# Performance work log

Hardware: AMD Instinct MI355X
Metric: run time of the kernel (lower is better)

The kernel has to match this reference:

```python
import jax, jax.numpy as jnp
import numpy as np

BITS = 4
MAXQ = 15            # 2**BITS - 1
PACK = 32 // BITS    # 8 int4 values per int32
GROUPSIZE = 128
M, K, N = 2048, 4096, 4096
G = K // GROUPSIZE


def setup_inputs() -> dict:
    key = jax.random.key(0)
    k1, k2, k3, k4, k5 = jax.random.split(key, 5)
    x = jax.random.normal(k1, (M, K), dtype=jnp.float32)
    qweight = jax.random.randint(k2, (K // PACK, N), 0, 2147483647, dtype=jnp.int32)
    qzeros = jax.random.randint(k3, (G, N // PACK), 0, 2147483647, dtype=jnp.int32)
    scales = jax.random.uniform(k4, (G, N), dtype=jnp.float32) * 0.01
    g_idx = (jnp.arange(K, dtype=jnp.int32) // GROUPSIZE).astype(jnp.int32)
    bias = jax.random.normal(k5, (N,), dtype=jnp.float32)
    return {"x": x, "qweight": qweight, "qzeros": qzeros,
            "scales": scales, "g_idx": g_idx, "bias": bias}


def _dequantize(qweight, qzeros, scales, g_idx):
    shifts = (jnp.arange(PACK, dtype=jnp.int32) * BITS)
    # unpack weights along K: [K//8, N] -> [K//8, 8, N] -> [K, N]
    w_int = ((qweight[:, None, :] >> shifts[None, :, None]) & MAXQ)
    w_int = w_int.reshape(K, N)
    # unpack zeros along N: [G, N//8] -> [G, N//8, 8] -> [G, N]; kernel adds 1
    z_int = ((qzeros[:, :, None] >> shifts[None, None, :]) & MAXQ) + 1
    z_int = z_int.reshape(G, N)
    # group-wise dequant: W[k, n] = (w - zeros[g_idx[k]]) * scales[g_idx[k]]
    W = (w_int - z_int[g_idx]).astype(jnp.float32) * scales[g_idx]
    return W  # [K, N]


def reference(x, qweight, qzeros, scales, g_idx, bias):
    W = _dequantize(qweight, qzeros, scales, g_idx)
    return x @ W + bias  # [M, N]
```

## Files before the change

kernel.cpp:

```cpp
#include <hip/hip_runtime.h>
#include <hip/hip_bf16.h>
#include <stdint.h>

#define M_DIM 2048
#define K_DIM 4096
#define N_DIM 4096

typedef __attribute__((ext_vector_type(8))) short short8;
typedef __attribute__((ext_vector_type(4))) float f32x4;

__device__ __forceinline__ uint32_t bf16pk(float a, float b) {
  uint32_t ua = __float_as_uint(a);
  ua = (ua + 0x7FFFu + ((ua >> 16) & 1u)) >> 16;
  uint32_t ub = __float_as_uint(b);
  ub = (ub + 0x7FFFu + ((ub >> 16) & 1u)) >> 16;
  return ua | (ub << 16);
}

__device__ __forceinline__ void glds16(const char* g, char* l) {
  __builtin_amdgcn_global_load_lds((__attribute__((address_space(1))) void*)g,
                                   (__attribute__((address_space(3))) void*)l, 16, 0, 0);
}


__global__ void __launch_bounds__(256) cvt_x_kernel(const float* __restrict__ x,
                                                    char* __restrict__ xImg) {
  const int mt = blockIdx.x >> 6, kt = blockIdx.x & 63;
  const int tid = threadIdx.x;
  const int k8 = tid & 7, rbase = tid >> 3;
  const float* xb = x + (size_t)mt * 256 * K_DIM + kt * 64 + k8 * 8;
  char* ob = xImg + (size_t)(mt * 64 + kt) * 32768 + k8 * 4096;
#pragma unroll
  for (int j = 0; j < 8; ++j) {
    int row = j * 32 + rbase;
    const float* src = xb + (size_t)row * K_DIM;
    float4 f0 = *(const float4*)src;
    float4 f1 = *(const float4*)(src + 4);
    uint4 pk;
    pk.x = bf16pk(f0.x, f0.y);
    pk.y = bf16pk(f0.z, f0.w);
    pk.z = bf16pk(f1.x, f1.y);
    pk.w = bf16pk(f1.z, f1.w);
    *(uint4*)(ob + row * 16) = pk;
  }
}

__global__ void __launch_bounds__(256) deq_w_kernel(const uint32_t* __restrict__ qweight,
                                                    const uint32_t* __restrict__ qzeros,
                                                    const float* __restrict__ scales,
                                                    char* __restrict__ wImg) {
  const int nt = blockIdx.x >> 6, kt = blockIdx.x & 63;
  const int t = threadIdx.x;
  const int n = nt * 256 + t;
  const int g = kt >> 1;
  uint32_t zq = qzeros[g * (N_DIM / 8) + (n >> 3)];
  const int z = (int)((zq >> ((n & 7) * 4)) & 15u) + 1;
  const float s = scales[g * N_DIM + n];
  char* ob = wImg + (size_t)(nt * 64 + kt) * 32768;
#pragma unroll
  for (int slot = 0; slot < 8; ++slot) {
    uint32_t q = qweight[(size_t)(kt * 8 + slot) * N_DIM + n];
    float f[8];
#pragma unroll
    for (int v = 0; v < 8; ++v) {
      int w = (int)((q >> (4 * v)) & 15u);
      f[v] = (float)(w - z) * s;
    }
    uint4 pk;
    pk.x = bf16pk(f[0], f[1]);
    pk.y = bf16pk(f[2], f[3]);
    pk.z = bf16pk(f[4], f[5]);
    pk.w = bf16pk(f[6], f[7]);
    *(uint4*)(ob + slot * 4096 + t * 16) = pk;
  }
}

__global__ void __launch_bounds__(512, 2) gemm_kernel(const char* __restrict__ xImg,
                                                      const char* __restrict__ wImg,
                                                      const float* __restrict__ bias,
                                                      float* __restrict__ out,
                                                      float* __restrict__ part1) {
  __shared__ uint4 ldsv[8192];
  char* lds = (char*)ldsv;
  const int tid = threadIdx.x;
  const int lane = tid & 63, wid = tid >> 6;
  const int wr = wid >> 2, wc = wid & 3;
  const int lr = lane & 15, lk = lane >> 4;

  const int bid = blockIdx.x;
  const int i5 = bid >> 3;
  const int nb = (bid & 7) * 2 + (i5 & 1);
  const int mb = (i5 >> 1) & 7;
  const int ks = i5 >> 4;

  f32x4 acc[8][4];
#pragma unroll
  for (int i = 0; i < 8; ++i)
#pragma unroll
    for (int j = 0; j < 4; ++j) acc[i][j] = f32x4{0.f, 0.f, 0.f, 0.f};

  const char* aT = xImg + (size_t)(mb * 64 + ks * 32) * 32768;
  const char* bT = wImg + (size_t)(nb * 64 + ks * 32) * 32768;

  int aoff[8], boff[4];
#pragma unroll
  for (int i = 0; i < 8; ++i) aoff[i] = lk * 4096 + (wr * 128 + i * 16 + lr) * 16;
#pragma unroll
  for (int j = 0; j < 4; ++j) boff[j] = 32768 + lk * 4096 + (wc * 64 + j * 16 + lr) * 16;

#define STG(src, off)                                        \
  do {                                                       \
    glds16((src) + tid * 16, lds + (off) + tid * 16);        \
    glds16((src) + 8192 + tid * 16, lds + (off) + 8192 + tid * 16); \
  } while (0)

  STG(aT, 0);
  STG(bT, 32768);
  STG(aT + 16384, 16384);
  STG(bT + 16384, 49152);
  STG(aT + 32768, 65536);
  STG(bT + 32768, 65536 + 32768);

#pragma unroll 2
  for (int t = 0; t < 32; ++t) {
    const int c = t & 1;
    char* bufc = lds + c * 65536;
    char* bufn = lds + (c ^ 1) * 65536;
    const char* aN1 = aT + (size_t)(t + 1) * 32768;
    const char* bN1 = bT + (size_t)(t + 1) * 32768;
    const char* aN2 = aT + (size_t)(t + 2) * 32768;
    const char* bN2 = bT + (size_t)(t + 2) * 32768;
    short8 a[8], b0, b1, b2, b3;

    if (t == 31) asm volatile("s_waitcnt vmcnt(4)" ::: "memory");
    else         asm volatile("s_waitcnt vmcnt(8)" ::: "memory");
    __builtin_amdgcn_sched_barrier(0);
    __builtin_amdgcn_s_barrier();
    if (t < 31) STG(aN1 + 16384, (c ^ 1) * 65536 + 16384);
#pragma unroll
    for (int i = 0; i < 8; ++i) a[i] = *(const short8*)(bufc + aoff[i]);
    b0 = *(const short8*)(bufc + boff[0]);
    b1 = *(const short8*)(bufc + boff[1]);
    __builtin_amdgcn_s_setprio(1);
#pragma unroll
    for (int i = 0; i < 8; ++i) {
      acc[i][0] = __builtin_amdgcn_mfma_f32_16x16x32_bf16(a[i], b0, acc[i][0], 0, 0, 0);
      acc[i][1] = __builtin_amdgcn_mfma_f32_16x16x32_bf16(a[i], b1, acc[i][1], 0, 0, 0);
    }
    __builtin_amdgcn_s_setprio(0);

    __builtin_amdgcn_s_barrier();
    if (t < 31) STG(bN1 + 16384, (c ^ 1) * 65536 + 32768 + 16384);
    b2 = *(const short8*)(bufc + boff[2]);
    b3 = *(const short8*)(bufc + boff[3]);
    __builtin_amdgcn_s_setprio(1);
#pragma unroll
    for (int i = 0; i < 8; ++i) {
      acc[i][2] = __builtin_amdgcn_mfma_f32_16x16x32_bf16(a[i], b2, acc[i][2], 0, 0, 0);
      acc[i][3] = __builtin_amdgcn_mfma_f32_16x16x32_bf16(a[i], b3, acc[i][3], 0, 0, 0);
    }
    __builtin_amdgcn_s_setprio(0);

    if (t == 31) asm volatile("s_waitcnt vmcnt(0)" ::: "memory");
    else         asm volatile("s_waitcnt vmcnt(8)" ::: "memory");
    __builtin_amdgcn_sched_barrier(0);
    __builtin_amdgcn_s_barrier();
    if (t < 30) STG(aN2, c * 65536);
#pragma unroll
    for (int i = 0; i < 8; ++i) a[i] = *(const short8*)(bufc + aoff[i] + 16384);
    b0 = *(const short8*)(bufc + boff[0] + 16384);
    b1 = *(const short8*)(bufc + boff[1] + 16384);
    __builtin_amdgcn_s_setprio(1);
#pragma unroll
    for (int i = 0; i < 8; ++i) {
      acc[i][0] = __builtin_amdgcn_mfma_f32_16x16x32_bf16(a[i], b0, acc[i][0], 0, 0, 0);
      acc[i][1] = __builtin_amdgcn_mfma_f32_16x16x32_bf16(a[i], b1, acc[i][1], 0, 0, 0);
    }
    __builtin_amdgcn_s_setprio(0);

    __builtin_amdgcn_s_barrier();
    if (t < 30) STG(bN2, c * 65536 + 32768);
    b2 = *(const short8*)(bufc + boff[2] + 16384);
    b3 = *(const short8*)(bufc + boff[3] + 16384);
    __builtin_amdgcn_s_setprio(1);
#pragma unroll
    for (int i = 0; i < 8; ++i) {
      acc[i][2] = __builtin_amdgcn_mfma_f32_16x16x32_bf16(a[i], b2, acc[i][2], 0, 0, 0);
      acc[i][3] = __builtin_amdgcn_mfma_f32_16x16x32_bf16(a[i], b3, acc[i][3], 0, 0, 0);
    }
    __builtin_amdgcn_s_setprio(0);
  }
#undef STG

  const int colB = nb * 256 + wc * 64 + lr;
  const int rowB = mb * 256 + wr * 128 + lk * 4;
  if (part1 != nullptr) {
    float* dst = ks ? part1 : out;
#pragma unroll
    for (int j = 0; j < 4; ++j) {
      int col = colB + j * 16;
      float bj = (ks == 0) ? bias[col] : 0.f;
#pragma unroll
      for (int i = 0; i < 8; ++i) {
        int row = rowB + i * 16;
#pragma unroll
        for (int r = 0; r < 4; ++r)
          dst[(size_t)(row + r) * N_DIM + col] = acc[i][j][r] + bj;
      }
    }
  } else {
#pragma unroll
    for (int j = 0; j < 4; ++j) {
      int col = colB + j * 16;
      float bj = (ks == 0) ? bias[col] : 0.f;
#pragma unroll
      for (int i = 0; i < 8; ++i) {
        int row = rowB + i * 16;
#pragma unroll
        for (int r = 0; r < 4; ++r)
          atomicAdd(&out[(size_t)(row + r) * N_DIM + col], acc[i][j][r] + bj);
      }
    }
  }
}

__global__ void __launch_bounds__(256) reduce_kernel(float* __restrict__ out,
                                                     const float* __restrict__ part1) {
  int i = blockIdx.x * 256 + threadIdx.x;
  float4 o = ((const float4*)out)[i];
  float4 p = ((const float4*)part1)[i];
  o.x += p.x; o.y += p.y; o.z += p.z; o.w += p.w;
  ((float4*)out)[i] = o;
}

__global__ void fallback_kernel(const float* __restrict__ x, const uint32_t* __restrict__ qweight,
                                const uint32_t* __restrict__ qzeros, const float* __restrict__ scales,
                                const float* __restrict__ bias, float* __restrict__ out) {
  __shared__ float xs[16][17];
  __shared__ float ws[16][17];
  int tx = threadIdx.x, ty = threadIdx.y;
  int col = blockIdx.x * 16 + tx;
  int row = blockIdx.y * 16 + ty;
  float acc = 0.f;
  for (int k0 = 0; k0 < K_DIM; k0 += 16) {
    xs[ty][tx] = x[(size_t)row * K_DIM + k0 + tx];
    int k = k0 + ty;
    int g = k >> 7;
    uint32_t q = qweight[(size_t)(k >> 3) * N_DIM + col];
    int w = (int)((q >> ((k & 7) * 4)) & 15u);
    uint32_t zq = qzeros[g * (N_DIM / 8) + (col >> 3)];
    int z = (int)((zq >> ((col & 7) * 4)) & 15u) + 1;
    ws[ty][tx] = (float)(w - z) * scales[g * N_DIM + col];
    __syncthreads();
#pragma unroll
    for (int kk = 0; kk < 16; ++kk) acc += xs[ty][kk] * ws[kk][tx];
    __syncthreads();
  }
  out[(size_t)row * N_DIM + col] = acc + bias[col];
}

extern "C" void kernel_launch(void* const* d_in, const int* in_sizes, int n_in,
                              void* d_out, int out_size, void* d_ws, size_t ws_size,
                              hipStream_t stream) {
  const float* x = (const float*)d_in[0];
  const uint32_t* qweight = (const uint32_t*)d_in[1];
  const uint32_t* qzeros = (const uint32_t*)d_in[2];
  const float* scales = (const float*)d_in[3];
  const float* bias = (const float*)d_in[5];
  float* out = (float*)d_out;

  const size_t X_IMG = (size_t)8 * 64 * 32768;
  const size_t W_IMG = (size_t)16 * 64 * 32768;
  const size_t PART = (size_t)M_DIM * N_DIM * 4;

  if (ws_size >= X_IMG + W_IMG + PART) {
    char* xImg = (char*)d_ws;
    char* wImg = (char*)d_ws + X_IMG;
    float* part1 = (float*)((char*)d_ws + X_IMG + W_IMG);
    cvt_x_kernel<<<512, 256, 0, stream>>>(x, xImg);
    deq_w_kernel<<<1024, 256, 0, stream>>>(qweight, qzeros, scales, wImg);
    gemm_kernel<<<256, 512, 0, stream>>>(xImg, wImg, bias, out, part1);
    reduce_kernel<<<8192, 256, 0, stream>>>(out, part1);
  } else if (ws_size >= X_IMG + W_IMG) {
    char* xImg = (char*)d_ws;
    char* wImg = (char*)d_ws + X_IMG;
    hipMemsetAsync(out, 0, (size_t)M_DIM * N_DIM * sizeof(float), stream);
    cvt_x_kernel<<<512, 256, 0, stream>>>(x, xImg);
    deq_w_kernel<<<1024, 256, 0, stream>>>(qweight, qzeros, scales, wImg);
    gemm_kernel<<<256, 512, 0, stream>>>(xImg, wImg, bias, out, nullptr);
  } else {
    fallback_kernel<<<dim3(N_DIM / 16, M_DIM / 16), dim3(16, 16), 0, stream>>>(
        x, qweight, qzeros, scales, bias, out);
  }
}
```

Baseline: 96.87 us.

## Restructure GEMM main loop into four-stage LDS ring with register-prefetched fragments

```diff
diff --git a/kernel.cpp b/kernel.cpp
--- a/kernel.cpp
+++ b/kernel.cpp
@@ -8,6 +8,8 @@
 
 typedef __attribute__((ext_vector_type(8))) short short8;
 typedef __attribute__((ext_vector_type(4))) float f32x4;
+
+#define MFMA __builtin_amdgcn_mfma_f32_16x16x32_bf16
 
 __device__ __forceinline__ uint32_t bf16pk(float a, float b) {
   uint32_t ua = __float_as_uint(a);
@@ -99,96 +101,115 @@
 #pragma unroll
     for (int j = 0; j < 4; ++j) acc[i][j] = f32x4{0.f, 0.f, 0.f, 0.f};
 
-  const char* aT = xImg + (size_t)(mb * 64 + ks * 32) * 32768;
-  const char* bT = wImg + (size_t)(nb * 64 + ks * 32) * 32768;
+  const char* aT = xImg + (size_t)(mb * 128 + ks * 64) * 16384;
+  const char* bT = wImg + (size_t)(nb * 128 + ks * 64) * 16384;
 
   int aoff[8], boff[4];
 #pragma unroll
   for (int i = 0; i < 8; ++i) aoff[i] = lk * 4096 + (wr * 128 + i * 16 + lr) * 16;
 #pragma unroll
-  for (int j = 0; j < 4; ++j) boff[j] = 32768 + lk * 4096 + (wc * 64 + j * 16 + lr) * 16;
-
-#define STG(src, off)                                        \
-  do {                                                       \
-    glds16((src) + tid * 16, lds + (off) + tid * 16);        \
-    glds16((src) + 8192 + tid * 16, lds + (off) + 8192 + tid * 16); \
+  for (int j = 0; j < 4; ++j) boff[j] = 16384 + lk * 4096 + (wc * 64 + j * 16 + lr) * 16;
+
+#define STG(src, dstoff)                                                 \
+  do {                                                                   \
+    glds16((src) + tid * 16, lds + (dstoff) + tid * 16);                 \
+    glds16((src) + 8192 + tid * 16, lds + (dstoff) + 8192 + tid * 16);   \
   } while (0)
 
-  STG(aT, 0);
-  STG(bT, 32768);
-  STG(aT + 16384, 16384);
-  STG(bT + 16384, 49152);
-  STG(aT + 32768, 65536);
-  STG(bT + 32768, 65536 + 32768);
-
-#pragma unroll 2
-  for (int t = 0; t < 32; ++t) {
-    const int c = t & 1;
-    char* bufc = lds + c * 65536;
-    char* bufn = lds + (c ^ 1) * 65536;
-    const char* aN1 = aT + (size_t)(t + 1) * 32768;
-    const char* bN1 = bT + (size_t)(t + 1) * 32768;
-    const char* aN2 = aT + (size_t)(t + 2) * 32768;
-    const char* bN2 = bT + (size_t)(t + 2) * 32768;
-    short8 a[8], b0, b1, b2, b3;
-
-    if (t == 31) asm volatile("s_waitcnt vmcnt(4)" ::: "memory");
-    else         asm volatile("s_waitcnt vmcnt(8)" ::: "memory");
+  STG(aT, 0);                STG(bT, 16384);
+  STG(aT + 16384, 32768);    STG(bT + 16384, 32768 + 16384);
+  STG(aT + 32768, 65536);    STG(bT + 32768, 65536 + 16384);
+  asm volatile("s_waitcnt vmcnt(8)" ::: "memory");
+  __builtin_amdgcn_sched_barrier(0);
+  __builtin_amdgcn_s_barrier();
+
+  short8 a0 = *(const short8*)(lds + aoff[0]);
+  short8 a1 = *(const short8*)(lds + aoff[1]);
+  short8 a2 = *(const short8*)(lds + aoff[2]);
+  short8 a3 = *(const short8*)(lds + aoff[3]);
+  short8 b0 = *(const short8*)(lds + boff[0]);
+  short8 b1 = *(const short8*)(lds + boff[1]);
+
+#pragma unroll 4
+  for (int t = 0; t < 64; ++t) {
+    const char* buf  = lds + (t & 3) * 32768;
+    const char* bufn = lds + ((t + 1) & 3) * 32768;
+    const int nso = ((t + 3) & 3) * 32768;
+    const char* aN = aT + (size_t)(t + 3) * 16384;
+    const char* bN = bT + (size_t)(t + 3) * 16384;
+
+    short8 b2 = *(const short8*)(buf + boff[2]);
+    short8 b3 = *(const short8*)(buf + boff[3]);
+    short8 a4 = *(const short8*)(buf + aoff[4]);
+    short8 a5 = *(const short8*)(buf + aoff[5]);
+    short8 a6 = *(const short8*)(buf + aoff[6]);
+    short8 a7 = *(const short8*)(buf + aoff[7]);
+    if (t <= 60) STG(aN, nso);
     __builtin_amdgcn_sched_barrier(0);
     __builtin_amdgcn_s_barrier();
-    if (t < 31) STG(aN1 + 16384, (c ^ 1) * 65536 + 16384);
-#pragma unroll
-    for (int i = 0; i < 8; ++i) a[i] = *(const short8*)(bufc + aoff[i]);
-    b0 = *(const short8*)(bufc + boff[0]);
-    b1 = *(const short8*)(bufc + boff[1]);
+    asm volatile("s_waitcnt lgkmcnt(6)" ::: "memory");
+    __builtin_amdgcn_sched_barrier(0);
     __builtin_amdgcn_s_setprio(1);
-#pragma unroll
-    for (int i = 0; i < 8; ++i) {
-      acc[i][0] = __builtin_amdgcn_mfma_f32_16x16x32_bf16(a[i], b0, acc[i][0], 0, 0, 0);
-      acc[i][1] = __builtin_amdgcn_mfma_f32_16x16x32_bf16(a[i], b1, acc[i][1], 0, 0, 0);
-    }
+    acc[0][0] = MFMA(a0, b0, acc[0][0], 0, 0, 0);
+    acc[1][0] = MFMA(a1, b0, acc[1][0], 0, 0, 0);
+    acc[2][0] = MFMA(a2, b0, acc[2][0], 0, 0, 0);
+    acc[3][0] = MFMA(a3, b0, acc[3][0], 0, 0, 0);
+    acc[0][1] = MFMA(a0, b1, acc[0][1], 0, 0, 0);
+    acc[1][1] = MFMA(a1, b1, acc[1][1], 0, 0, 0);
+    acc[2][1] = MFMA(a2, b1, acc[2][1], 0, 0, 0);
+    acc[3][1] = MFMA(a3, b1, acc[3][1], 0, 0, 0);
+    asm volatile("s_waitcnt lgkmcnt(4)" ::: "memory");
+    __builtin_amdgcn_sched_barrier(0);
+    acc[0][2] = MFMA(a0, b2, acc[0][2], 0, 0, 0);
+    acc[1][2] = MFMA(a1, b2, acc[1][2], 0, 0, 0);
+    acc[2][2] = MFMA(a2, b2, acc[2][2], 0, 0, 0);
+    acc[3][2] = MFMA(a3, b2, acc[3][2], 0, 0, 0);
+    acc[0][3] = MFMA(a0, b3, acc[0][3], 0, 0, 0);
+    acc[1][3] = MFMA(a1, b3, acc[1][3], 0, 0, 0);
+    acc[2][3] = MFMA(a2, b3, acc[2][3], 0, 0, 0);
+    acc[3][3] = MFMA(a3, b3, acc[3][3], 0, 0, 0);
     __builtin_amdgcn_s_setprio(0);
-
+    if (t <= 60)      asm volatile("s_waitcnt vmcnt(6)" ::: "memory");
+    else if (t == 61) asm volatile("s_waitcnt vmcnt(4)" ::: "memory");
+    else if (t == 62) asm volatile("s_waitcnt vmcnt(0)" ::: "memory");
+    __builtin_amdgcn_sched_barrier(0);
     __builtin_amdgcn_s_barrier();
-    if (t < 31) STG(bN1 + 16384, (c ^ 1) * 65536 + 32768 + 16384);
-    b2 = *(const short8*)(bufc + boff[2]);
-    b3 = *(const short8*)(bufc + boff[3]);
+    __builtin_amdgcn_sched_barrier(0);
+
+    short8 na0 = *(const short8*)(bufn + aoff[0]);
+    short8 na1 = *(const short8*)(bufn + aoff[1]);
+    short8 na2 = *(const short8*)(bufn + aoff[2]);
+    short8 na3 = *(const short8*)(bufn + aoff[3]);
+    short8 nb0 = *(const short8*)(bufn + boff[0]);
+    short8 nb1 = *(const short8*)(bufn + boff[1]);
+    if (t <= 60) STG(bN, nso + 16384);
+    __builtin_amdgcn_sched_barrier(0);
+    __builtin_amdgcn_s_barrier();
+    asm volatile("s_waitcnt lgkmcnt(6)" ::: "memory");
+    __builtin_amdgcn_sched_barrier(0);
     __builtin_amdgcn_s_setprio(1);
-#pragma unroll
-    for (int i = 0; i < 8; ++i) {
-      acc[i][2] = __builtin_amdgcn_mfma_f32_16x16x32_bf16(a[i], b2, acc[i][2], 0, 0, 0);
-      acc[i][3] = __builtin_amdgcn_mfma_f32_16x16x32_bf16(a[i], b3, acc[i][3], 0, 0, 0);
-    }
+    acc[4][0] = MFMA(a4, b0, acc[4][0], 0, 0, 0);
+    acc[5][0] = MFMA(a5, b0, acc[5][0], 0, 0, 0);
+    acc[6][0] = MFMA(a6, b0, acc[6][0], 0, 0, 0);
+    acc[7][0] = MFMA(a7, b0, acc[7][0], 0, 0, 0);
+    acc[4][1] = MFMA(a4, b1, acc[4][1], 0, 0, 0);
+    acc[5][1] = MFMA(a5, b1, acc[5][1], 0, 0, 0);
+    acc[6][1] = MFMA(a6, b1, acc[6][1], 0, 0, 0);
+    acc[7][1] = MFMA(a7, b1, acc[7][1], 0, 0, 0);
+    acc[4][2] = MFMA(a4, b2, acc[4][2], 0, 0, 0);
+    acc[5][2] = MFMA(a5, b2, acc[5][2], 0, 0, 0);
+    acc[6][2] = MFMA(a6, b2, acc[6][2], 0, 0, 0);
+    acc[7][2] = MFMA(a7, b2, acc[7][2], 0, 0, 0);
+    acc[4][3] = MFMA(a4, b3, acc[4][3], 0, 0, 0);
+    acc[5][3] = MFMA(a5, b3, acc[5][3], 0, 0, 0);
+    acc[6][3] = MFMA(a6, b3, acc[6][3], 0, 0, 0);
+    acc[7][3] = MFMA(a7, b3, acc[7][3], 0, 0, 0);
     __builtin_amdgcn_s_setprio(0);
-
-    if (t == 31) asm volatile("s_waitcnt vmcnt(0)" ::: "memory");
-    else         asm volatile("s_waitcnt vmcnt(8)" ::: "memory");
     __builtin_amdgcn_sched_barrier(0);
     __builtin_amdgcn_s_barrier();
-    if (t < 30) STG(aN2, c * 65536);
-#pragma unroll
-    for (int i = 0; i < 8; ++i) a[i] = *(const short8*)(bufc + aoff[i] + 16384);
-    b0 = *(const short8*)(bufc + boff[0] + 16384);
-    b1 = *(const short8*)(bufc + boff[1] + 16384);
-    __builtin_amdgcn_s_setprio(1);
-#pragma unroll
-    for (int i = 0; i < 8; ++i) {
-      acc[i][0] = __builtin_amdgcn_mfma_f32_16x16x32_bf16(a[i], b0, acc[i][0], 0, 0, 0);
-      acc[i][1] = __builtin_amdgcn_mfma_f32_16x16x32_bf16(a[i], b1, acc[i][1], 0, 0, 0);
-    }
-    __builtin_amdgcn_s_setprio(0);
-
-    __builtin_amdgcn_s_barrier();
-    if (t < 30) STG(bN2, c * 65536 + 32768);
-    b2 = *(const short8*)(bufc + boff[2] + 16384);
-    b3 = *(const short8*)(bufc + boff[3] + 16384);
-    __builtin_amdgcn_s_setprio(1);
-#pragma unroll
-    for (int i = 0; i < 8; ++i) {
-      acc[i][2] = __builtin_amdgcn_mfma_f32_16x16x32_bf16(a[i], b2, acc[i][2], 0, 0, 0);
-      acc[i][3] = __builtin_amdgcn_mfma_f32_16x16x32_bf16(a[i], b3, acc[i][3], 0, 0, 0);
-    }
-    __builtin_amdgcn_s_setprio(0);
+    __builtin_amdgcn_sched_barrier(0);
+
+    a0 = na0; a1 = na1; a2 = na2; a3 = na3; b0 = nb0; b1 = nb1;
   }
 #undef STG
 
@@ -279,7 +300,7 @@
     float* part1 = (float*)((char*)d_ws + X_IMG + W_IMG);
     cvt_x_kernel<<<512, 256, 0, stream>>>(x, xImg);
     deq_w_kernel<<<1024, 256, 0, stream>>>(qweight, qzeros, scales, wImg);
-    gemm_kernel<<<256, 512, 0, stream>>>(xImg, wImg, bias, out, part1);
+    gemm_kernel<<<256, 512, 0, stream>>>((const char*)xImg, (const char*)wImg, bias, out, part1);
     reduce_kernel<<<8192, 256, 0, stream>>>(out, part1);
   } else if (ws_size >= X_IMG + W_IMG) {
     char* xImg = (char*)d_ws;
@@ -287,7 +308,7 @@
     hipMemsetAsync(out, 0, (size_t)M_DIM * N_DIM * sizeof(float), stream);
     cvt_x_kernel<<<512, 256, 0, stream>>>(x, xImg);
     deq_w_kernel<<<1024, 256, 0, stream>>>(qweight, qzeros, scales, wImg);
-    gemm_kernel<<<256, 512, 0, stream>>>(xImg, wImg, bias, out, nullptr);
+    gemm_kernel<<<256, 512, 0, stream>>>((const char*)xImg, (const char*)wImg, bias, out, nullptr);
   } else {
     fallback_kernel<<<dim3(N_DIM / 16, M_DIM / 16), dim3(16, 16), 0, stream>>>(
         x, qweight, qzeros, scales, bias, out);
```

New measurement: 100.3 us. 1.04x slower.
